# Kernel optimization log

Hardware: AMD Instinct MI355X
Metric: run time of the kernel (lower is better)

## Reference

```python
import jax, jax.numpy as jnp
import numpy as np

B, S, OBS, ZD, HID, T, PD = 256, 512, 64, 16, 256, 64, 2
ITERS, ELITES = 4, 64
SMOOTH, STD_FLOOR = 0.25, 0.2
IW, AW, RW = 1.0, 0.5, 1.0


def setup_inputs() -> dict:
    key = jax.random.key(0)
    ks = jax.random.split(key, 32)
    f32 = jnp.float32

    def w(k, shape):
        return jax.random.normal(k, shape, f32) / np.float32(np.sqrt(shape[0]))

    return {
        "s0": jax.random.normal(ks[0], (B, OBS), f32),
        "eps": jax.random.normal(ks[1], (ITERS, B, S, ZD), f32),
        "enc_w1": w(ks[2], (OBS, HID)), "enc_b1": jnp.zeros((HID,), f32),
        "enc_w2": w(ks[3], (HID, HID)), "enc_b2": jnp.zeros((HID,), f32),
        "zmu_w": w(ks[4], (HID, ZD)), "zmu_b": jnp.zeros((ZD,), f32),
        "zls_w": w(ks[5], (HID, ZD)), "zls_b": jnp.zeros((ZD,), f32),
        "mu_w1": w(ks[6], (OBS + ZD, HID)), "mu_b1": jnp.zeros((HID,), f32),
        "mu_w2": w(ks[7], (HID, HID)), "mu_b2": jnp.zeros((HID,), f32),
        "mu_w3": w(ks[8], (HID, T * PD)), "mu_b3": jnp.zeros((T * PD,), f32),
        "sig_w1": w(ks[9], (ZD, HID)), "sig_b1": jnp.zeros((HID,), f32),
        "sig_w2": w(ks[10], (HID, HID)), "sig_b2": jnp.zeros((HID,), f32),
        "sig_w3": w(ks[11], (HID, T * PD)), "sig_b3": jnp.zeros((T * PD,), f32),  # bias zero-init per nn.init.zeros_
        "risk_w1": w(ks[12], (OBS + ZD, HID)), "risk_b1": jnp.zeros((HID,), f32),
        "risk_w2": w(ks[13], (HID, HID)), "risk_b2": jnp.zeros((HID,), f32),
        "risk_w3": w(ks[14], (HID, 1)), "risk_b3": jnp.zeros((1,), f32),
    }


def _cem_bind(s0, eps, enc_w1, enc_b1, enc_w2, enc_b2, zmu_w, zmu_b, zls_w, zls_b,
              mu_w1, mu_b1, mu_w2, mu_b2, mu_w3, mu_b3,
              sig_w1, sig_b1, sig_w2, sig_b2, sig_w3, sig_b3,
              risk_w1, risk_b1, risk_w2, risk_b2, risk_w3, risk_b3):
    relu = jax.nn.relu
    b, obs = s0.shape
    iters, _, s, zd = eps.shape

    # --- TubeNet.encode: q(z|s0) ---
    h = relu(s0 @ enc_w1 + enc_b1)
    h = relu(h @ enc_w2 + enc_b2)
    mu = h @ zmu_w + zmu_b                                   # [B, ZD]
    std = jnp.exp(jnp.clip(h @ zls_w + zls_b, -4.0, 2.0))    # [B, ZD]

    goal = s0[:, 2:4]                                        # extract_goal
    s0e = jnp.broadcast_to(s0[:, None, :], (b, s, obs))      # [B, S, OBS]

    best_score = jnp.full((b,), -jnp.inf, dtype=s0.dtype)
    best_z = mu

    for i in range(iters):  # small fixed CEM iteration count
        z = mu[:, None, :] + std[:, None, :] * eps[i]        # [B, S, ZD]
        x = jnp.concatenate([s0e, z], axis=-1)               # [B, S, OBS+ZD]

        # predict_tube: mu_net(s0, z)
        hm = relu(x @ mu_w1 + mu_b1)
        hm = relu(hm @ mu_w2 + mu_b2)
        mu_out = (hm @ mu_w3 + mu_b3).reshape(b, s, T, PD)

        # sigma_net(z), clamp(-4, 3); agency = -mean(log sigma) = -mean(logsig)
        hs = relu(z @ sig_w1 + sig_b1)
        hs = relu(hs @ sig_w2 + sig_b2)
        logsig = jnp.clip(hs @ sig_w3 + sig_b3, -4.0, 3.0)   # [B, S, T*PD]

        # intent proxy: ||mu_T - goal||^2
        intent = jnp.sum((mu_out[:, :, -1, :] - goal[:, None, :]) ** 2, axis=-1)  # [B, S]
        agency = -jnp.mean(logsig, axis=-1)                  # [B, S]

        # RiskNet(s0, z)
        hr = relu(x @ risk_w1 + risk_b1)
        hr = relu(hr @ risk_w2 + risk_b2)
        risk = jax.nn.sigmoid(hr @ risk_w3 + risk_b3)[..., 0]  # [B, S]

        score = -IW * intent + AW * agency - RW * risk       # [B, S]

        vals, idx = jax.lax.top_k(score, ELITES)             # [B, E]
        elite_z = jnp.take_along_axis(z, idx[:, :, None], axis=1)  # [B, E, ZD]

        better = vals[:, 0] > best_score
        top_z = jnp.take_along_axis(z, idx[:, :1, None], axis=1)[:, 0, :]
        best_score = jnp.where(better, vals[:, 0], best_score)
        best_z = jnp.where(better[:, None], top_z, best_z)

        new_mu = elite_z.mean(axis=1)
        new_std = jnp.std(elite_z, axis=1, ddof=1)           # torch .std default (unbiased)
        mu = SMOOTH * mu + (1.0 - SMOOTH) * new_mu
        std = jnp.maximum(SMOOTH * std + (1.0 - SMOOTH) * new_std, STD_FLOOR)

    return jnp.concatenate([best_z, best_score[:, None]], axis=-1)  # [B, ZD+1]


def reference(s0, eps, enc_w1, enc_b1, enc_w2, enc_b2, zmu_w, zmu_b, zls_w, zls_b,
              mu_w1, mu_b1, mu_w2, mu_b2, mu_w3, mu_b3,
              sig_w1, sig_b1, sig_w2, sig_b2, sig_w3, sig_b3,
              risk_w1, risk_b1, risk_w2, risk_b2, risk_w3, risk_b3):
    return _cem_bind(s0, eps, enc_w1, enc_b1, enc_w2, enc_b2, zmu_w, zmu_b, zls_w, zls_b,
                     mu_w1, mu_b1, mu_w2, mu_b2, mu_w3, mu_b3,
                     sig_w1, sig_b1, sig_w2, sig_b2, sig_w3, sig_b3,
                     risk_w1, risk_b1, risk_w2, risk_b2, risk_w3, risk_b3)
```

## Files before the change

kernel.cpp:

```cpp
#include <hip/hip_runtime.h>

#define B_    256
#define S_    512
#define OBS_  64
#define ZD_   16
#define HID_  256
#define ITERS_ 4
#define RT_   32
#define STRH_ 36

__global__ __launch_bounds__(256) void enc_kernel(
    const float* __restrict__ s0,
    const float* __restrict__ w1, const float* __restrict__ b1,
    const float* __restrict__ w2, const float* __restrict__ b2,
    const float* __restrict__ zmw, const float* __restrict__ zmb,
    const float* __restrict__ zlw, const float* __restrict__ zlb,
    const float* __restrict__ mu_w1, const float* __restrict__ mu_b1,
    const float* __restrict__ risk_w1, const float* __restrict__ risk_b1,
    float* __restrict__ mu, float* __restrict__ stdv, float* __restrict__ bscore,
    float* __restrict__ base_mu, float* __restrict__ base_risk)
{
    __shared__ float s0s[OBS_];
    __shared__ float h1[HID_];
    __shared__ float h2[HID_];
    const int b = blockIdx.x, tid = threadIdx.x;
    if (tid < OBS_) s0s[tid] = s0[b * OBS_ + tid];
    __syncthreads();
    {
        float am = mu_b1[tid], ar = risk_b1[tid];
        for (int k = 0; k < OBS_; ++k) {
            am = fmaf(s0s[k], mu_w1[k * 256 + tid], am);
            ar = fmaf(s0s[k], risk_w1[k * 256 + tid], ar);
        }
        base_mu[b * 256 + tid]   = am;
        base_risk[b * 256 + tid] = ar;
    }
    float a = b1[tid];
    for (int k = 0; k < OBS_; ++k) a = fmaf(s0s[k], w1[k * HID_ + tid], a);
    h1[tid] = fmaxf(a, 0.f);
    __syncthreads();
    float a2 = b2[tid];
    for (int k = 0; k < HID_; ++k) a2 = fmaf(h1[k], w2[k * HID_ + tid], a2);
    h2[tid] = fmaxf(a2, 0.f);
    __syncthreads();
    if (tid < ZD_) {
        float m = zmb[tid];
        for (int k = 0; k < HID_; ++k) m = fmaf(h2[k], zmw[k * ZD_ + tid], m);
        mu[b * ZD_ + tid] = m;
    } else if (tid < 2 * ZD_) {
        const int d = tid - ZD_;
        float l = zlb[d];
        for (int k = 0; k < HID_; ++k) l = fmaf(h2[k], zlw[k * ZD_ + d], l);
        l = fminf(fmaxf(l, -4.f), 2.f);
        stdv[b * ZD_ + d] = expf(l);
    } else if (tid == 2 * ZD_) {
        bscore[b] = -INFINITY;
    }
}

__device__ __forceinline__ void fma16x2(
    const float* __restrict__ row, float wx, float wy,
    float* __restrict__ acc0, float* __restrict__ acc1)
{
    const float4 a0 = *(const float4*)(row);
    const float4 a1 = *(const float4*)(row + 4);
    const float4 a2 = *(const float4*)(row + 8);
    const float4 a3 = *(const float4*)(row + 12);
    const float aa[16] = {a0.x,a0.y,a0.z,a0.w, a1.x,a1.y,a1.z,a1.w,
                          a2.x,a2.y,a2.z,a2.w, a3.x,a3.y,a3.z,a3.w};
#pragma unroll
    for (int r = 0; r < 16; ++r) {
        acc0[r] = fmaf(aa[r], wx, acc0[r]);
        acc1[r] = fmaf(aa[r], wy, acc1[r]);
    }
}

__device__ __forceinline__ void fma16x1(
    const float* __restrict__ row, float w, float* __restrict__ acc)
{
    const float4 a0 = *(const float4*)(row);
    const float4 a1 = *(const float4*)(row + 4);
    const float4 a2 = *(const float4*)(row + 8);
    const float4 a3 = *(const float4*)(row + 12);
    const float aa[16] = {a0.x,a0.y,a0.z,a0.w, a1.x,a1.y,a1.z,a1.w,
                          a2.x,a2.y,a2.z,a2.w, a3.x,a3.y,a3.z,a3.w};
#pragma unroll
    for (int r = 0; r < 16; ++r) acc[r] = fmaf(aa[r], w, acc[r]);
}

__device__ __forceinline__ void gemm_k2(
    const float* __restrict__ inS, int K,
    const float* __restrict__ wcol,
    float* __restrict__ acc0, float* __restrict__ acc1)
{
    float2 wA[4], wB[4];
#pragma unroll
    for (int i = 0; i < 4; ++i) wA[i] = *(const float2*)(wcol + (size_t)i * 256);
#pragma unroll 1
    for (int k0 = 0; k0 < K; k0 += 8) {
#pragma unroll
        for (int i = 0; i < 4; ++i)
            wB[i] = *(const float2*)(wcol + (size_t)(k0 + 4 + i) * 256);
#pragma unroll
        for (int i = 0; i < 4; ++i)
            fma16x2(inS + (k0 + i) * STRH_, wA[i].x, wA[i].y, acc0, acc1);
        if (k0 + 8 < K) {
#pragma unroll
            for (int i = 0; i < 4; ++i)
                wA[i] = *(const float2*)(wcol + (size_t)(k0 + 8 + i) * 256);
        }
#pragma unroll
        for (int i = 0; i < 4; ++i)
            fma16x2(inS + (k0 + 4 + i) * STRH_, wB[i].x, wB[i].y, acc0, acc1);
    }
}

__device__ __forceinline__ void gemm_k1(
    const float* __restrict__ inS, int K,
    const float* __restrict__ wcol, int wstride, float* __restrict__ acc)
{
    float wA[4], wB[4];
#pragma unroll
    for (int i = 0; i < 4; ++i) wA[i] = wcol[(size_t)i * wstride];
#pragma unroll 1
    for (int k0 = 0; k0 < K; k0 += 8) {
#pragma unroll
        for (int i = 0; i < 4; ++i) wB[i] = wcol[(size_t)(k0 + 4 + i) * wstride];
#pragma unroll
        for (int i = 0; i < 4; ++i) fma16x1(inS + (k0 + i) * STRH_, wA[i], acc);
        if (k0 + 8 < K) {
#pragma unroll
            for (int i = 0; i < 4; ++i) wA[i] = wcol[(size_t)(k0 + 8 + i) * wstride];
        }
#pragma unroll
        for (int i = 0; i < 4; ++i) fma16x1(inS + (k0 + 4 + i) * STRH_, wB[i], acc);
    }
}

__device__ __forceinline__ void store16_relu(float* __restrict__ dst, int c,
                                             int g16, const float* __restrict__ acc)
{
#pragma unroll
    for (int q = 0; q < 4; ++q) {
        float4 o;
        o.x = fmaxf(acc[4*q+0], 0.f); o.y = fmaxf(acc[4*q+1], 0.f);
        o.z = fmaxf(acc[4*q+2], 0.f); o.w = fmaxf(acc[4*q+3], 0.f);
        *(float4*)(dst + (size_t)c * STRH_ + g16 + 4*q) = o;
    }
}

__global__ __launch_bounds__(256, 4) void score_kernel(
    const float* __restrict__ s0, const float* __restrict__ eps,
    const float* __restrict__ mu_w1,
    const float* __restrict__ mu_w2, const float* __restrict__ mu_b2,
    const float* __restrict__ mu_w3, const float* __restrict__ mu_b3,
    const float* __restrict__ sig_w1, const float* __restrict__ sig_b1,
    const float* __restrict__ sig_w2, const float* __restrict__ sig_b2,
    const float* __restrict__ sig_w3, const float* __restrict__ sig_b3,
    const float* __restrict__ risk_w1,
    const float* __restrict__ risk_w2, const float* __restrict__ risk_b2,
    const float* __restrict__ risk_w3, const float* __restrict__ risk_b3,
    const float* __restrict__ base_mu, const float* __restrict__ base_risk,
    const float* __restrict__ mu, const float* __restrict__ stdv,
    float* __restrict__ score, int iter)
{
    __shared__ __align__(16) float zT[ZD_ * STRH_];
    __shared__ __align__(16) float h[HID_ * STRH_];
    __shared__ float red[4][RT_], red2[4][RT_];
    __shared__ float intentL[RT_], agencyL[RT_];
    __shared__ float muS[ZD_], stdS[ZD_];

    const int tid  = threadIdx.x;
    const int g    = tid >> 7;
    const int g16  = g * 16;
    const int c0   = (tid & 127) * 2;
    const int row0 = blockIdx.x * RT_;
    const int b    = row0 >> 9;

    if (tid < ZD_) { muS[tid] = mu[b * ZD_ + tid]; stdS[tid] = stdv[b * ZD_ + tid]; }
    __syncthreads();
    {
        const float* epsI = eps + ((size_t)iter * B_ * S_ + row0) * ZD_;
        for (int l = tid; l < RT_ * ZD_; l += 256) {
            const int r = l & 31, d = l >> 5;
            zT[d * STRH_ + r] = fmaf(stdS[d], epsI[r * ZD_ + d], muS[d]);
        }
    }
    __syncthreads();

    float acc0[16], acc1[16];

    {
        const float2 bm = *(const float2*)(base_mu + (size_t)b * 256 + c0);
#pragma unroll
        for (int r = 0; r < 16; ++r) { acc0[r] = bm.x; acc1[r] = bm.y; }
        gemm_k2(zT + g16, ZD_, mu_w1 + (size_t)OBS_ * 256 + c0, acc0, acc1);
        store16_relu(h, c0, g16, acc0); store16_relu(h, c0 + 1, g16, acc1);
    }
    __syncthreads();
    {
        const float2 bv = *(const float2*)(mu_b2 + c0);
#pragma unroll
        for (int r = 0; r < 16; ++r) { acc0[r] = bv.x; acc1[r] = bv.y; }
        gemm_k2(h + g16, HID_, mu_w2 + c0, acc0, acc1);
    }
    __syncthreads();
    store16_relu(h, c0, g16, acc0); store16_relu(h, c0 + 1, g16, acc1);
    __syncthreads();
    {
        const int r = tid & 31, seg = tid >> 5, w = tid >> 6;
        float p0 = 0.f, p1 = 0.f;
        for (int i = 0; i < 32; ++i) {
            const int k = seg * 32 + i;
            const float hv = h[k * STRH_ + r];
            const float2 wv = *(const float2*)(mu_w3 + (size_t)k * 128 + 126);
            p0 = fmaf(hv, wv.x, p0);
            p1 = fmaf(hv, wv.y, p1);
        }
        p0 += __shfl_xor(p0, 32);
        p1 += __shfl_xor(p1, 32);
        if ((tid & 32) == 0) { red[w][r] = p0; red2[w][r] = p1; }
    }
    {
        const float2 bv = *(const float2*)(sig_b1 + c0);
#pragma unroll
        for (int r = 0; r < 16; ++r) { acc0[r] = bv.x; acc1[r] = bv.y; }
        gemm_k2(zT + g16, ZD_, sig_w1 + c0, acc0, acc1);
    }
    __syncthreads();
    store16_relu(h, c0, g16, acc0); store16_relu(h, c0 + 1, g16, acc1);
    if (tid < RT_) {
        float m0 = red[0][tid] + red[1][tid] + red[2][tid] + red[3][tid] + mu_b3[126];
        float m1 = red2[0][tid] + red2[1][tid] + red2[2][tid] + red2[3][tid] + mu_b3[127];
        const float g0 = s0[b * OBS_ + 2], g1 = s0[b * OBS_ + 3];
        const float d0 = m0 - g0, d1 = m1 - g1;
        intentL[tid] = d0 * d0 + d1 * d1;
    }
    __syncthreads();
    {
        const float2 bv = *(const float2*)(sig_b2 + c0);
#pragma unroll
        for (int r = 0; r < 16; ++r) { acc0[r] = bv.x; acc1[r] = bv.y; }
        gemm_k2(h + g16, HID_, sig_w2 + c0, acc0, acc1);
    }
    __syncthreads();
    store16_relu(h, c0, g16, acc0); store16_relu(h, c0 + 1, g16, acc1);
    __syncthreads();
    {
        const int c = tid & 127;
        float acc[16];
        const float bv = sig_b3[c];
#pragma unroll
        for (int r = 0; r < 16; ++r) acc[r] = bv;
        gemm_k1(h + g16, HID_, sig_w3 + c, 128, acc);
        __syncthreads();
#pragma unroll
        for (int q = 0; q < 4; ++q) {
            float4 o;
            o.x = fminf(fmaxf(acc[4*q+0], -4.f), 3.f);
            o.y = fminf(fmaxf(acc[4*q+1], -4.f), 3.f);
            o.z = fminf(fmaxf(acc[4*q+2], -4.f), 3.f);
            o.w = fminf(fmaxf(acc[4*q+3], -4.f), 3.f);
            *(float4*)(h + (size_t)c * STRH_ + g16 + 4*q) = o;
        }
    }
    __syncthreads();
    {
        const int r = tid & 31, seg = tid >> 5, w = tid >> 6;
        float s = 0.f;
        for (int i = 0; i < 16; ++i) s += h[(seg * 16 + i) * STRH_ + r];
        s += __shfl_xor(s, 32);
        if ((tid & 32) == 0) red[w][r] = s;
    }
    {
        const float2 bm = *(const float2*)(base_risk + (size_t)b * 256 + c0);
#pragma unroll
        for (int r = 0; r < 16; ++r) { acc0[r] = bm.x; acc1[r] = bm.y; }
        gemm_k2(zT + g16, ZD_, risk_w1 + (size_t)OBS_ * 256 + c0, acc0, acc1);
    }
    __syncthreads();
    store16_relu(h, c0, g16, acc0); store16_relu(h, c0 + 1, g16, acc1);
    if (tid < RT_) {
        const float s = red[0][tid] + red[1][tid] + red[2][tid] + red[3][tid];
        agencyL[tid] = -s * (1.f / 128.f);
    }
    __syncthreads();
    {
        const float2 bv = *(const float2*)(risk_b2 + c0);
#pragma unroll
        for (int r = 0; r < 16; ++r) { acc0[r] = bv.x; acc1[r] = bv.y; }
        gemm_k2(h + g16, HID_, risk_w2 + c0, acc0, acc1);
    }
    __syncthreads();
    store16_relu(h, c0, g16, acc0); store16_relu(h, c0 + 1, g16, acc1);
    __syncthreads();
    {
        const int r = tid & 31, seg = tid >> 5, w = tid >> 6;
        float p = 0.f;
        for (int i = 0; i < 32; ++i) {
            const int k = seg * 32 + i;
            p = fmaf(h[k * STRH_ + r], risk_w3[k], p);
        }
        p += __shfl_xor(p, 32);
        if ((tid & 32) == 0) red[w][r] = p;
    }
    __syncthreads();
    if (tid < RT_) {
        const float p = red[0][tid] + red[1][tid] + red[2][tid] + red[3][tid];
        const float risk = 1.f / (1.f + expf(-(p + risk_b3[0])));
        score[row0 + tid] = -intentL[tid] + 0.5f * agencyL[tid] - risk;
    }
}

__global__ __launch_bounds__(256) void update_kernel(
    const float* __restrict__ score, const float* __restrict__ eps,
    float* __restrict__ mu, float* __restrict__ stdv,
    float* __restrict__ bscore, float* __restrict__ bz, int iter)
{
    __shared__ unsigned long long keys[512];
    __shared__ float ez[64][ZD_];
    __shared__ float mold[ZD_], sold[ZD_];
    __shared__ int flagL, idx0L;

    const int b = blockIdx.x, tid = threadIdx.x;

    for (int l = tid; l < 512; l += 256) {
        const float sc = score[b * 512 + l];
        unsigned int u = __float_as_uint(sc);
        u = (u & 0x80000000u) ? ~u : (u | 0x80000000u);
        const unsigned long long key =
            ((unsigned long long)u << 32) | (unsigned long long)(511 - l);
        keys[l] = ~key;
    }
    if (tid < ZD_) { mold[tid] = mu[b * ZD_ + tid]; sold[tid] = stdv[b * ZD_ + tid]; }
    __syncthreads();

    for (int size = 2; size < 512; size <<= 1) {
        const int ddd = ((tid & (size >> 1)) != 0) ? 0 : 1;
        for (int stride = size >> 1; stride > 0; stride >>= 1) {
            __syncthreads();
            const int pos = 2 * tid - (tid & (stride - 1));
            const unsigned long long a = keys[pos], c = keys[pos + stride];
            if ((a > c) == (ddd != 0)) { keys[pos] = c; keys[pos + stride] = a; }
        }
    }
    for (int stride = 256; stride > 0; stride >>= 1) {
        __syncthreads();
        const int pos = 2 * tid - (tid & (stride - 1));
        const unsigned long long a = keys[pos], c = keys[pos + stride];
        if (a > c) { keys[pos] = c; keys[pos + stride] = a; }
    }
    __syncthreads();

    const float* epsB = eps + ((size_t)iter * B_ * S_ + (size_t)b * S_) * ZD_;
    for (int l = tid; l < 64 * ZD_; l += 256) {
        const int e = l >> 4, d = l & 15;
        const unsigned long long key = ~keys[e];
        const int idx = 511 - (int)(key & 0xFFFFFFFFull);
        ez[e][d] = fmaf(sold[d], epsB[idx * ZD_ + d], mold[d]);
    }
    __syncthreads();

    if (tid < ZD_) {
        float s = 0.f;
        for (int e = 0; e < 64; ++e) s += ez[e][tid];
        const float mean = s * (1.f / 64.f);
        float v = 0.f;
        for (int e = 0; e < 64; ++e) { const float d = ez[e][tid] - mean; v = fmaf(d, d, v); }
        const float sd = sqrtf(v * (1.f / 63.f));
        mu[b * ZD_ + tid]   = 0.25f * mold[tid] + 0.75f * mean;
        stdv[b * ZD_ + tid] = fmaxf(0.25f * sold[tid] + 0.75f * sd, 0.2f);
    }
    if (tid == 0) {
        const unsigned long long key = ~keys[0];
        const int idx0 = 511 - (int)(key & 0xFFFFFFFFull);
        const float v = score[b * 512 + idx0];
        const int better = (v > bscore[b]) ? 1 : 0;
        if (better) bscore[b] = v;
        flagL = better; idx0L = idx0;
    }
    __syncthreads();
    if (tid < ZD_ && flagL)
        bz[b * ZD_ + tid] = fmaf(sold[tid], epsB[idx0L * ZD_ + tid], mold[tid]);
}

__global__ __launch_bounds__(256) void out_kernel(
    const float* __restrict__ bz, const float* __restrict__ bscore,
    float* __restrict__ out)
{
    const int i = blockIdx.x * 256 + threadIdx.x;
    if (i < B_ * 17) {
        const int b = i / 17, d = i % 17;
        out[i] = (d < ZD_) ? bz[b * ZD_ + d] : bscore[b];
    }
}

extern "C" void kernel_launch(void* const* d_in, const int* in_sizes, int n_in,
                              void* d_out, int out_size, void* d_ws, size_t ws_size,
                              hipStream_t stream)
{
    (void)in_sizes; (void)n_in; (void)out_size; (void)ws_size;
    const float* s0      = (const float*)d_in[0];
    const float* eps     = (const float*)d_in[1];
    const float* enc_w1  = (const float*)d_in[2];
    const float* enc_b1  = (const float*)d_in[3];
    const float* enc_w2  = (const float*)d_in[4];
    const float* enc_b2  = (const float*)d_in[5];
    const float* zmu_w   = (const float*)d_in[6];
    const float* zmu_b   = (const float*)d_in[7];
    const float* zls_w   = (const float*)d_in[8];
    const float* zls_b   = (const float*)d_in[9];
    const float* mu_w1   = (const float*)d_in[10];
    const float* mu_b1   = (const float*)d_in[11];
    const float* mu_w2   = (const float*)d_in[12];
    const float* mu_b2   = (const float*)d_in[13];
    const float* mu_w3   = (const float*)d_in[14];
    const float* mu_b3   = (const float*)d_in[15];
    const float* sig_w1  = (const float*)d_in[16];
    const float* sig_b1  = (const float*)d_in[17];
    const float* sig_w2  = (const float*)d_in[18];
    const float* sig_b2  = (const float*)d_in[19];
    const float* sig_w3  = (const float*)d_in[20];
    const float* sig_b3  = (const float*)d_in[21];
    const float* risk_w1 = (const float*)d_in[22];
    const float* risk_b1 = (const float*)d_in[23];
    const float* risk_w2 = (const float*)d_in[24];
    const float* risk_b2 = (const float*)d_in[25];
    const float* risk_w3 = (const float*)d_in[26];
    const float* risk_b3 = (const float*)d_in[27];

    float* ws        = (float*)d_ws;
    float* mu        = ws;
    float* stdv      = ws + 4096;
    float* bscore    = ws + 8192;
    float* bz        = ws + 8448;
    float* score     = ws + 12544;
    float* base_mu   = ws + 143616;
    float* base_risk = ws + 209152;

    enc_kernel<<<B_, 256, 0, stream>>>(s0, enc_w1, enc_b1, enc_w2, enc_b2,
                                       zmu_w, zmu_b, zls_w, zls_b,
                                       mu_w1, mu_b1, risk_w1, risk_b1,
                                       mu, stdv, bscore, base_mu, base_risk);
    for (int it = 0; it < ITERS_; ++it) {
        score_kernel<<<(B_ * S_) / RT_, 256, 0, stream>>>(
            s0, eps,
            mu_w1, mu_w2, mu_b2, mu_w3, mu_b3,
            sig_w1, sig_b1, sig_w2, sig_b2, sig_w3, sig_b3,
            risk_w1, risk_w2, risk_b2, risk_w3, risk_b3,
            base_mu, base_risk,
            mu, stdv, score, it);
        update_kernel<<<B_, 256, 0, stream>>>(score, eps, mu, stdv, bscore, bz, it);
    }
    out_kernel<<<(B_ * 17 + 255) / 256, 256, 0, stream>>>(bz, bscore,
                                                          (float*)d_out);
}
```

Before: 3.330 ms.

## Double score-kernel row tile to 64 rows with 512-thread blocks

Each score_kernel block now processes 64 sample rows with 512 threads instead of 32 rows with 256. Every weight element loaded for the MLP layers is reused across twice as many rows. The reductions are rewritten for 8 row segments without shuffles, and the eps load is reindexed to be contiguous, which should improve coalescing. The larger LDS tile (about 74KB per block) and the bigger block may limit how many blocks fit per CU, and the grid halves.

```diff
diff --git a/kernel.cpp b/kernel.cpp
--- a/kernel.cpp
+++ b/kernel.cpp
@@ -6,8 +6,8 @@
 #define ZD_   16
 #define HID_  256
 #define ITERS_ 4
-#define RT_   32
-#define STRH_ 36
+#define RT_   64
+#define STRH_ 68
 
 __global__ __launch_bounds__(256) void enc_kernel(
     const float* __restrict__ s0,
@@ -149,7 +149,7 @@
     }
 }
 
-__global__ __launch_bounds__(256, 4) void score_kernel(
+__global__ __launch_bounds__(512, 4) void score_kernel(
     const float* __restrict__ s0, const float* __restrict__ eps,
     const float* __restrict__ mu_w1,
     const float* __restrict__ mu_w2, const float* __restrict__ mu_b2,
@@ -166,7 +166,7 @@
 {
     __shared__ __align__(16) float zT[ZD_ * STRH_];
     __shared__ __align__(16) float h[HID_ * STRH_];
-    __shared__ float red[4][RT_], red2[4][RT_];
+    __shared__ float red[8][RT_], red2[8][RT_];
     __shared__ float intentL[RT_], agencyL[RT_];
     __shared__ float muS[ZD_], stdS[ZD_];
 
@@ -181,9 +181,9 @@
     __syncthreads();
     {
         const float* epsI = eps + ((size_t)iter * B_ * S_ + row0) * ZD_;
-        for (int l = tid; l < RT_ * ZD_; l += 256) {
-            const int r = l & 31, d = l >> 5;
-            zT[d * STRH_ + r] = fmaf(stdS[d], epsI[r * ZD_ + d], muS[d]);
+        for (int l = tid; l < RT_ * ZD_; l += 512) {
+            const int r = l >> 4, d = l & 15;
+            zT[d * STRH_ + r] = fmaf(stdS[d], epsI[l], muS[d]);
         }
     }
     __syncthreads();
@@ -208,7 +208,7 @@
     store16_relu(h, c0, g16, acc0); store16_relu(h, c0 + 1, g16, acc1);
     __syncthreads();
     {
-        const int r = tid & 31, seg = tid >> 5, w = tid >> 6;
+        const int r = tid & 63, seg = tid >> 6;
         float p0 = 0.f, p1 = 0.f;
         for (int i = 0; i < 32; ++i) {
             const int k = seg * 32 + i;
@@ -217,9 +217,7 @@
             p0 = fmaf(hv, wv.x, p0);
             p1 = fmaf(hv, wv.y, p1);
         }
-        p0 += __shfl_xor(p0, 32);
-        p1 += __shfl_xor(p1, 32);
-        if ((tid & 32) == 0) { red[w][r] = p0; red2[w][r] = p1; }
+        red[seg][r] = p0; red2[seg][r] = p1;
     }
     {
         const float2 bv = *(const float2*)(sig_b1 + c0);
@@ -230,8 +228,9 @@
     __syncthreads();
     store16_relu(h, c0, g16, acc0); store16_relu(h, c0 + 1, g16, acc1);
     if (tid < RT_) {
-        float m0 = red[0][tid] + red[1][tid] + red[2][tid] + red[3][tid] + mu_b3[126];
-        float m1 = red2[0][tid] + red2[1][tid] + red2[2][tid] + red2[3][tid] + mu_b3[127];
+        float m0 = mu_b3[126], m1 = mu_b3[127];
+#pragma unroll
+        for (int sg = 0; sg < 8; ++sg) { m0 += red[sg][tid]; m1 += red2[sg][tid]; }
         const float g0 = s0[b * OBS_ + 2], g1 = s0[b * OBS_ + 3];
         const float d0 = m0 - g0, d1 = m1 - g1;
         intentL[tid] = d0 * d0 + d1 * d1;
@@ -266,11 +265,10 @@
     }
     __syncthreads();
     {
-        const int r = tid & 31, seg = tid >> 5, w = tid >> 6;
+        const int r = tid & 63, seg = tid >> 6;
         float s = 0.f;
         for (int i = 0; i < 16; ++i) s += h[(seg * 16 + i) * STRH_ + r];
-        s += __shfl_xor(s, 32);
-        if ((tid & 32) == 0) red[w][r] = s;
+        red[seg][r] = s;
     }
     {
         const float2 bm = *(const float2*)(base_risk + (size_t)b * 256 + c0);
@@ -281,7 +279,9 @@
     __syncthreads();
     store16_relu(h, c0, g16, acc0); store16_relu(h, c0 + 1, g16, acc1);
     if (tid < RT_) {
-        const float s = red[0][tid] + red[1][tid] + red[2][tid] + red[3][tid];
+        float s = 0.f;
+#pragma unroll
+        for (int sg = 0; sg < 8; ++sg) s += red[sg][tid];
         agencyL[tid] = -s * (1.f / 128.f);
     }
     __syncthreads();
@@ -295,18 +295,19 @@
     store16_relu(h, c0, g16, acc0); store16_relu(h, c0 + 1, g16, acc1);
     __syncthreads();
     {
-        const int r = tid & 31, seg = tid >> 5, w = tid >> 6;
+        const int r = tid & 63, seg = tid >> 6;
         float p = 0.f;
         for (int i = 0; i < 32; ++i) {
             const int k = seg * 32 + i;
             p = fmaf(h[k * STRH_ + r], risk_w3[k], p);
         }
-        p += __shfl_xor(p, 32);
-        if ((tid & 32) == 0) red[w][r] = p;
+        red[seg][r] = p;
     }
     __syncthreads();
     if (tid < RT_) {
-        const float p = red[0][tid] + red[1][tid] + red[2][tid] + red[3][tid];
+        float p = 0.f;
+#pragma unroll
+        for (int sg = 0; sg < 8; ++sg) p += red[sg][tid];
         const float risk = 1.f / (1.f + expf(-(p + risk_b3[0])));
         score[row0 + tid] = -intentL[tid] + 0.5f * agencyL[tid] - risk;
     }
@@ -443,7 +444,7 @@
                                        mu_w1, mu_b1, risk_w1, risk_b1,
                                        mu, stdv, bscore, base_mu, base_risk);
     for (int it = 0; it < ITERS_; ++it) {
-        score_kernel<<<(B_ * S_) / RT_, 256, 0, stream>>>(
+        score_kernel<<<(B_ * S_) / RT_, 512, 0, stream>>>(
             s0, eps,
             mu_w1, mu_w2, mu_b2, mu_w3, mu_b3,
             sig_w1, sig_b1, sig_w2, sig_b2, sig_w3, sig_b3,
```

Result: slower. 3.568 ms (+7.1%).
